# Kernel optimization log

Hardware: AMD Instinct MI355X
Metric: run time of the kernel (lower is better)

The kernel has to match this reference:

```python
import jax, jax.numpy as jnp
from jax import lax
import numpy as np

THRESHOLD = 1.25
CURRENT_DECAY = 0.25
VOLTAGE_DECAY = 0.03
TAU_GRAD = 0.03
SCALE_GRAD = 3.0


@jax.custom_vjp
def spike_fn(v):
    # Heaviside spike on membrane voltage (threshold already subtracted)
    return (v >= 0.0).astype(v.dtype)

def _spike_fwd(v):
    return spike_fn(v), v

def _spike_bwd(v, g):
    # slayer-style exponential surrogate gradient around threshold
    surrogate = SCALE_GRAD * jnp.exp(-jnp.abs(v) / TAU_GRAD)
    return (g * surrogate,)

spike_fn.defvjp(_spike_fwd, _spike_bwd)


def cuba_dense(x, v_w, g_w, delay):
    """x: [B, C_in, T] spikes -> [B, C_out, T] spikes.
    Weight-normalized dense synapse + CUBA leaky-integrate-and-fire scan + axonal delay."""
    # weight norm: W = g * v / ||v||_row
    norm = jnp.sqrt(jnp.sum(v_w * v_w, axis=1, keepdims=True))
    W = g_w[:, None] * v_w / norm                       # [O, C]
    z = jnp.einsum('bct,oc->bot', x, W)                 # synaptic current input [B, O, T]
    B, O, T = z.shape
    zT = jnp.transpose(z, (2, 0, 1))                    # [T, B, O]

    def step(carry, zt):
        cur, vol = carry
        cur = cur * (1.0 - CURRENT_DECAY) + zt
        vol = vol * (1.0 - VOLTAGE_DECAY) + cur
        s = spike_fn(vol - THRESHOLD)
        vol = vol * (1.0 - s)                           # reset to zero on spike
        return (cur, vol), s

    init = (jnp.zeros((B, O), z.dtype), jnp.zeros((B, O), z.dtype))
    _, sT = lax.scan(step, init, zT)                    # [T, B, O]
    s = jnp.transpose(sT, (1, 2, 0))                    # [B, O, T]

    # per-neuron integer axonal delay: out[b,n,t] = s[b,n,t-d_n]
    t_idx = jnp.arange(T)[None, :] - delay[:, None]     # [O, T]
    valid = (t_idx >= 0)
    gathered = s[:, jnp.arange(O)[:, None], jnp.clip(t_idx, 0, T - 1)]
    return jnp.where(valid[None, :, :], gathered, jnp.zeros((), s.dtype))


def setup_inputs() -> dict:
    key = jax.random.key(0)
    ks = jax.random.split(key, 10)
    B, C, T = 32, 34 * 34 * 2, 300
    spike = (jax.random.uniform(ks[0], (B, C, T)) < 0.1).astype(jnp.float32)
    v1 = jax.random.normal(ks[1], (512, C), jnp.float32) * 0.1
    g1 = jax.random.uniform(ks[2], (512,), jnp.float32) + 0.5
    v2 = jax.random.normal(ks[3], (512, 512), jnp.float32) * 0.1
    g2 = jax.random.uniform(ks[4], (512,), jnp.float32) + 0.5
    v3 = jax.random.normal(ks[5], (10, 512), jnp.float32) * 0.1
    g3 = jax.random.uniform(ks[6], (10,), jnp.float32) + 0.5
    d1 = jax.random.randint(ks[7], (512,), 0, 8, jnp.int32)
    d2 = jax.random.randint(ks[8], (512,), 0, 8, jnp.int32)
    d3 = jax.random.randint(ks[9], (10,), 0, 8, jnp.int32)
    return {"spike": spike, "v1": v1, "g1": g1, "v2": v2, "g2": g2,
            "v3": v3, "g3": g3, "d1": d1, "d2": d2, "d3": d3}


def reference(spike, v1, g1, v2, g2, v3, g3, d1, d2, d3):
    s1 = cuba_dense(spike, v1, g1, d1)
    s2 = cuba_dense(s1, v2, g2, d2)
    s3 = cuba_dense(s2, v3, g3, d3)
    counts = jnp.stack([jnp.mean(s1), jnp.mean(s2), jnp.mean(s3)]).reshape(1, -1)
    return s3, counts
```

## Files before the change

kernel.cpp:

```cpp
#include <hip/hip_runtime.h>

#define B_   32
#define T_   300
#define C1_  2312
#define O1_  512
#define O2_  512
#define O3_  10
#define M_   (B_*T_)
#define KSPLIT_ 1152


__global__ void calc_f(const float* __restrict__ v, const float* __restrict__ g,
                       double* __restrict__ f, int O, int C) {
    int o = blockIdx.x;
    const float* row = v + (size_t)o * C;
    double s = 0.0;
    for (int c = threadIdx.x; c < C; c += blockDim.x) {
        double x = (double)row[c];
        s += x * x;
    }
    for (int off = 32; off; off >>= 1) s += __shfl_down(s, off);
    __shared__ double wsum[4];
    int lane = threadIdx.x & 63, wv = threadIdx.x >> 6;
    if (lane == 0) wsum[wv] = s;
    __syncthreads();
    if (threadIdx.x == 0) {
        double tot = 0.0;
        for (int i = 0; i < (int)(blockDim.x >> 6); ++i) tot += wsum[i];
        f[o] = (double)g[o] / sqrt(tot);
    }
}

__global__ void transpose_scale(const float* __restrict__ v, const double* __restrict__ f,
                                double* __restrict__ wt, int O, int C, int ldo) {
    __shared__ double tile[32][33];
    int c0 = blockIdx.x * 32, o0 = blockIdx.y * 32;
    int tx = threadIdx.x, ty = threadIdx.y;
    for (int k = 0; k < 4; ++k) {
        int o = o0 + ty + k * 8, c = c0 + tx;
        double val = 0.0;
        if (o < O && c < C) val = (double)v[(size_t)o * C + c] * f[o];
        tile[ty + k * 8][tx] = val;
    }
    __syncthreads();
    for (int k = 0; k < 4; ++k) {
        int c = c0 + ty + k * 8, o = o0 + tx;
        if (c < C && o < O) wt[(size_t)c * ldo + o] = tile[tx][ty + k * 8];
    }
}

__global__ void build_bits(const float* __restrict__ X, unsigned* __restrict__ bits) {
    size_t idx = (size_t)blockIdx.x * 256 + threadIdx.x;
    if (idx >= (size_t)B_ * C1_ * 10) return;
    int t32 = (int)(idx % 10);
    size_t bc = idx / 10;
    const float* src = X + bc * T_ + t32 * 32;
    int nq = (t32 == 9) ? 3 : 8;
    unsigned m = 0;
    for (int q = 0; q < nq; ++q) {
        float4 v = *(const float4*)(src + q * 4);
        if (v.x != 0.f) m |= 1u << (q * 4 + 0);
        if (v.y != 0.f) m |= 1u << (q * 4 + 1);
        if (v.z != 0.f) m |= 1u << (q * 4 + 2);
        if (v.w != 0.f) m |= 1u << (q * 4 + 3);
    }
    bits[idx] = m;
}

__global__ __launch_bounds__(256) void gemm1(const unsigned* __restrict__ Xbits,
                                             const double* __restrict__ Wt,
                                             double* __restrict__ Z) {
    __shared__ double Ws[16][256];
    int zb = blockIdx.z;
    int b = zb >> 1, khalf = zb & 1;
    int cbeg = khalf ? KSPLIT_ : 0;
    const int NT = khalf ? 73 : 72;
    int o0 = blockIdx.y * 256;
    int tb = blockIdx.x;
    int tid = threadIdx.x;
    int lane = tid & 63;
    int w8s = __builtin_amdgcn_readfirstlane((tid >> 6) << 3);
    double acc[8][4];
#pragma unroll
    for (int tj = 0; tj < 8; ++tj)
#pragma unroll
        for (int i = 0; i < 4; ++i) acc[tj][i] = 0.0;
    const unsigned* xbp = Xbits + (size_t)b * C1_ * 10 + tb;

    double2 wreg[8];
    unsigned mk[16], mkn[16];

    auto load_w = [&](int c0) {
#pragma unroll
        for (int h = 0; h < 8; ++h) {
            int idx = h * 256 + tid;
            int i = idx >> 7, od = (idx & 127) * 2;
            int c = c0 + i;
            double2 val; val.x = 0.0; val.y = 0.0;
            if (c < C1_) val = *(const double2*)(Wt + (size_t)c * O1_ + o0 + od);
            wreg[h] = val;
        }
    };
    auto load_m = [&](unsigned* dst, int c0) {
#pragma unroll
        for (int k = 0; k < 16; ++k) {
            int c = c0 + k;
            dst[k] = (c < C1_) ? xbp[(size_t)c * 10] : 0u;
        }
    };
    auto store_w = [&]() {
#pragma unroll
        for (int h = 0; h < 8; ++h) {
            int idx = h * 256 + tid;
            int i = idx >> 7, od = (idx & 127) * 2;
            *(double2*)(&Ws[i][od]) = wreg[h];
        }
    };

    load_w(cbeg);
    load_m(mk, cbeg);
    for (int tile = 0; tile < NT; ++tile) {
        store_w();
        __syncthreads();
        if (tile + 1 < NT) {
            int cn = cbeg + (tile + 1) * 16;
            load_w(cn);
            load_m(mkn, cn);
        }
#pragma unroll
        for (int k = 0; k < 16; ++k) {
            unsigned smk = (unsigned)__builtin_amdgcn_readfirstlane((int)mk[k]);
            unsigned soct = (smk >> w8s) & 0xffu;
            if (soct) {
                double wf[4];
#pragma unroll
                for (int i = 0; i < 4; ++i) wf[i] = Ws[k][lane + 64 * i];
#pragma unroll
                for (int tj = 0; tj < 8; ++tj) {
                    if (soct & (1u << tj)) {
#pragma unroll
                        for (int i = 0; i < 4; ++i) acc[tj][i] += wf[i];
                    }
                }
            }
        }
#pragma unroll
        for (int k = 0; k < 16; ++k) mk[k] = mkn[k];
        __syncthreads();
    }
#pragma unroll
    for (int tj = 0; tj < 8; ++tj) {
        int t = tb * 32 + w8s + tj;
        if (t < T_) {
            double* dst = Z + ((size_t)b * T_ + t) * O1_ + o0;
#pragma unroll
            for (int i = 0; i < 4; ++i)
                atomicAdd(&dst[lane + 64 * i], acc[tj][i]);
        }
    }
}

__global__ __launch_bounds__(256) void gemm2(const float* __restrict__ A,
                                             const double* __restrict__ Wt,
                                             double* __restrict__ Z) {
    __shared__ double Ws[16][128];
    __shared__ double As[64][17];
    int m0 = blockIdx.x * 64;
    int o0 = blockIdx.y * 128;
    int tid = threadIdx.x;
    int to = tid & 15, tm = tid >> 4;
    double acc[8][4];
#pragma unroll
    for (int i = 0; i < 8; ++i)
#pragma unroll
        for (int j = 0; j < 4; ++j) acc[i][j] = 0.0;
    for (int c0 = 0; c0 < 512; c0 += 16) {
        {
            int m = tid >> 2, ch = (tid & 3) * 4;
            float4 v = *(const float4*)(A + (size_t)(m0 + m) * 512 + c0 + ch);
            As[m][ch + 0] = (double)v.x; As[m][ch + 1] = (double)v.y;
            As[m][ch + 2] = (double)v.z; As[m][ch + 3] = (double)v.w;
        }
#pragma unroll
        for (int h = 0; h < 4; ++h) {
            int idx = h * 512 + tid * 2;
            int i = idx >> 7, o = idx & 127;
            *(double2*)(&Ws[i][o]) = *(const double2*)(Wt + (size_t)(c0 + i) * 512 + o0 + o);
        }
        __syncthreads();
#pragma unroll
        for (int k = 0; k < 16; ++k) {
            double wf[8], xf[4];
#pragma unroll
            for (int i = 0; i < 8; ++i) wf[i] = Ws[k][to + 16 * i];
#pragma unroll
            for (int j = 0; j < 4; ++j) xf[j] = As[tm * 4 + j][k];
#pragma unroll
            for (int i = 0; i < 8; ++i)
#pragma unroll
                for (int j = 0; j < 4; ++j) acc[i][j] = fma(wf[i], xf[j], acc[i][j]);
        }
        __syncthreads();
    }
#pragma unroll
    for (int j = 0; j < 4; ++j) {
        double* dst = Z + (size_t)(m0 + tm * 4 + j) * 512 + o0;
#pragma unroll
        for (int i = 0; i < 8; ++i) dst[to + 16 * i] = acc[i][j];
    }
}

__global__ __launch_bounds__(256) void gemm3(const float* __restrict__ A,
                                             const double* __restrict__ Wt,
                                             double* __restrict__ Z) {
    __shared__ double w[512 * 16];
    for (int e = threadIdx.x; e < 4096; e += 256)
        ((double2*)w)[e] = ((const double2*)Wt)[e];
    __syncthreads();
    int m = blockIdx.x * 256 + threadIdx.x;
    if (m >= M_) return;
    double acc[O3_];
#pragma unroll
    for (int o = 0; o < O3_; ++o) acc[o] = 0.0;
    const float4* Ar = (const float4*)(A + (size_t)m * 512);
    for (int cq = 0; cq < 128; ++cq) {
        float4 a = Ar[cq];
        float av[4] = {a.x, a.y, a.z, a.w};
#pragma unroll
        for (int u = 0; u < 4; ++u)
#pragma unroll
            for (int o = 0; o < O3_; ++o) acc[o] += (double)av[u] * w[(cq * 4 + u) * 16 + o];
    }
    double* dst = Z + (size_t)m * 16;
#pragma unroll
    for (int o = 0; o < O3_; ++o) dst[o] = acc[o];
}

__global__ void scan12(const double* __restrict__ Zin,
                       const int* __restrict__ delay,
                       float* __restrict__ Sout,
                       float* __restrict__ sumOut) {
    int blk = blockIdx.x;
    int o = (blk & 7) * 64 + threadIdx.x;
    int b = blk >> 3;
    const double* z = Zin + (size_t)b * T_ * O1_ + o;
    float* s = Sout + (size_t)b * T_ * O1_ + o;
    int d = delay[o];
    for (int t = 0; t < d; ++t) s[(size_t)t * O1_] = 0.f;
    double cur = 0.0, vol = 0.0;
    float cnt = 0.f;
    for (int t8 = 0; t8 < 296; t8 += 8) {
        double zb[8];
#pragma unroll
        for (int u = 0; u < 8; ++u) zb[u] = z[(size_t)(t8 + u) * O1_];
#pragma unroll
        for (int u = 0; u < 8; ++u) {
            int t = t8 + u;
            cur = cur * 0.75 + zb[u];
            vol = vol * 0.97 + cur;
            float sp = (vol >= 1.25) ? 1.f : 0.f;
            if (sp > 0.f) vol = 0.0;
            int tw = t + d;
            if (tw < T_) { s[(size_t)tw * O1_] = sp; cnt += sp; }
        }
    }
    {
        double zb[4];
#pragma unroll
        for (int u = 0; u < 4; ++u) zb[u] = z[(size_t)(296 + u) * O1_];
#pragma unroll
        for (int u = 0; u < 4; ++u) {
            int t = 296 + u;
            cur = cur * 0.75 + zb[u];
            vol = vol * 0.97 + cur;
            float sp = (vol >= 1.25) ? 1.f : 0.f;
            if (sp > 0.f) vol = 0.0;
            int tw = t + d;
            if (tw < T_) { s[(size_t)tw * O1_] = sp; cnt += sp; }
        }
    }
    for (int off = 32; off; off >>= 1) cnt += __shfl_down(cnt, off);
    if (threadIdx.x == 0) atomicAdd(sumOut, cnt);
}

__global__ void scan3(const double* __restrict__ Z3,
                      const int* __restrict__ d3,
                      float* __restrict__ out,
                      float* __restrict__ sumOut) {
    __shared__ double zt[T_ * 16];
    int b = blockIdx.x;
    const double2* src = (const double2*)(Z3 + (size_t)b * T_ * 16);
    for (int e = threadIdx.x; e < T_ * 8; e += 64)
        ((double2*)zt)[e] = src[e];
    __syncthreads();
    int o = threadIdx.x;
    if (o < O3_) {
        int d = d3[o];
        float* dst = out + (size_t)b * O3_ * T_ + (size_t)o * T_;
        for (int t = 0; t < d; ++t) dst[t] = 0.f;
        double cur = 0.0, vol = 0.0;
        float cnt = 0.f;
        for (int t = 0; t < T_; ++t) {
            cur = cur * 0.75 + zt[t * 16 + o];
            vol = vol * 0.97 + cur;
            float sp = (vol >= 1.25) ? 1.f : 0.f;
            if (sp > 0.f) vol = 0.0;
            int tw = t + d;
            if (tw < T_) { dst[tw] = sp; cnt += sp; }
        }
        atomicAdd(sumOut, cnt);
    }
}

__global__ void finalize(const float* __restrict__ sums, float* __restrict__ out) {
    if (threadIdx.x == 0) {
        out[0] = (float)((double)sums[0] / (double)(B_ * O1_ * T_));
        out[1] = (float)((double)sums[1] / (double)(B_ * O2_ * T_));
        out[2] = (float)((double)sums[2] / (double)(B_ * O3_ * T_));
    }
}

extern "C" void kernel_launch(void* const* d_in, const int* in_sizes, int n_in,
                              void* d_out, int out_size, void* d_ws, size_t ws_size,
                              hipStream_t stream) {
    const float* spike = (const float*)d_in[0];
    const float* v1 = (const float*)d_in[1];
    const float* g1 = (const float*)d_in[2];
    const float* v2 = (const float*)d_in[3];
    const float* g2 = (const float*)d_in[4];
    const float* v3 = (const float*)d_in[5];
    const float* g3 = (const float*)d_in[6];
    const int* d1 = (const int*)d_in[7];
    const int* d2 = (const int*)d_in[8];
    const int* d3 = (const int*)d_in[9];
    float* out = (float*)d_out;

    double* dw = (double*)d_ws;
    size_t off = 0;
    double* f1  = dw + off; off += 512;
    double* f2  = dw + off; off += 512;
    double* f3  = dw + off; off += 16;
    double* Wt1 = dw + off; off += (size_t)C1_ * O1_;
    double* Wt2 = dw + off; off += 512 * 512;
    double* Wt3 = dw + off; off += 512 * 16;
    double* zA  = dw + off; off += (size_t)M_ * 512;
    double* z3b = dw + off; off += (size_t)M_ * 16;
    float* fw = (float*)(dw + off);
    float* sB    = fw;
    float* sums  = fw + (size_t)M_ * 512;
    unsigned* Xbits = (unsigned*)(fw + (size_t)M_ * 512 + 4);
    (void)ws_size; (void)out_size; (void)in_sizes; (void)n_in;

    hipMemsetAsync(sums, 0, 4 * sizeof(float), stream);
    hipMemsetAsync(zA, 0, (size_t)M_ * 512 * sizeof(double), stream);

    build_bits<<<(B_ * C1_ * 10 + 255) / 256, 256, 0, stream>>>(spike, Xbits);

    calc_f<<<512, 256, 0, stream>>>(v1, g1, f1, O1_, C1_);
    calc_f<<<512, 256, 0, stream>>>(v2, g2, f2, O2_, O1_);
    calc_f<<<O3_, 256, 0, stream>>>(v3, g3, f3, O3_, O2_);

    transpose_scale<<<dim3((C1_ + 31) / 32, 16), dim3(32, 8), 0, stream>>>(v1, f1, Wt1, O1_, C1_, O1_);
    transpose_scale<<<dim3(16, 16), dim3(32, 8), 0, stream>>>(v2, f2, Wt2, O2_, O1_, O2_);
    transpose_scale<<<dim3(16, 1), dim3(32, 8), 0, stream>>>(v3, f3, Wt3, O3_, O2_, 16);

    gemm1<<<dim3(10, 2, B_ * 2), 256, 0, stream>>>(Xbits, Wt1, zA);
    scan12<<<256, 64, 0, stream>>>(zA, d1, sB, sums + 0);
    gemm2<<<dim3(M_ / 64, 4), 256, 0, stream>>>(sB, Wt2, zA);
    scan12<<<256, 64, 0, stream>>>(zA, d2, sB, sums + 1);
    gemm3<<<(M_ + 255) / 256, 256, 0, stream>>>(sB, Wt3, z3b);
    scan3<<<B_, 64, 0, stream>>>(z3b, d3, out, sums + 2);
    finalize<<<1, 64, 0, stream>>>(sums, out + (size_t)B_ * O3_ * T_);
}
```

Before: 854.2 us.

## Bit-pack layer-1 spikes and make gemm2 a sparse masked accumulation

The layer-1 scan now writes its spikes as 32-bit time masks per neuron instead of dense float rows. The second-layer GEMM reads these masks and, for each input channel and group of 8 timesteps, adds weight rows only where a spike bit is set. This replaces dense fp64 FMAs with conditional adds, mirroring the existing gemm1 design. It also software-pipelines the weight and mask loads across tiles, at the cost of wave-uniform branching and more register use.

```diff
diff --git a/kernel.cpp b/kernel.cpp
--- a/kernel.cpp
+++ b/kernel.cpp
@@ -160,53 +160,86 @@
     }
 }
 
-__global__ __launch_bounds__(256) void gemm2(const float* __restrict__ A,
+__global__ __launch_bounds__(256) void gemm2(const unsigned* __restrict__ Sbits,
                                              const double* __restrict__ Wt,
                                              double* __restrict__ Z) {
-    __shared__ double Ws[16][128];
-    __shared__ double As[64][17];
-    int m0 = blockIdx.x * 64;
-    int o0 = blockIdx.y * 128;
+    __shared__ double Ws[16][256];
+    int b  = blockIdx.z;
+    int o0 = blockIdx.y * 256;
+    int tb = blockIdx.x;
     int tid = threadIdx.x;
-    int to = tid & 15, tm = tid >> 4;
+    int lane = tid & 63;
+    int w8s = __builtin_amdgcn_readfirstlane((tid >> 6) << 3);
     double acc[8][4];
 #pragma unroll
-    for (int i = 0; i < 8; ++i)
-#pragma unroll
-        for (int j = 0; j < 4; ++j) acc[i][j] = 0.0;
-    for (int c0 = 0; c0 < 512; c0 += 16) {
-        {
-            int m = tid >> 2, ch = (tid & 3) * 4;
-            float4 v = *(const float4*)(A + (size_t)(m0 + m) * 512 + c0 + ch);
-            As[m][ch + 0] = (double)v.x; As[m][ch + 1] = (double)v.y;
-            As[m][ch + 2] = (double)v.z; As[m][ch + 3] = (double)v.w;
-        }
-#pragma unroll
-        for (int h = 0; h < 4; ++h) {
-            int idx = h * 512 + tid * 2;
-            int i = idx >> 7, o = idx & 127;
-            *(double2*)(&Ws[i][o]) = *(const double2*)(Wt + (size_t)(c0 + i) * 512 + o0 + o);
-        }
+    for (int tj = 0; tj < 8; ++tj)
+#pragma unroll
+        for (int i = 0; i < 4; ++i) acc[tj][i] = 0.0;
+    const unsigned* xbp = Sbits + (size_t)b * 512 * 10 + tb;
+
+    double2 wreg[8];
+    unsigned mk[16], mkn[16];
+
+    auto load_w = [&](int c0) {
+#pragma unroll
+        for (int h = 0; h < 8; ++h) {
+            int idx = h * 256 + tid;
+            int i = idx >> 7, od = (idx & 127) * 2;
+            wreg[h] = *(const double2*)(Wt + (size_t)(c0 + i) * 512 + o0 + od);
+        }
+    };
+    auto load_m = [&](unsigned* dst, int c0) {
+#pragma unroll
+        for (int k = 0; k < 16; ++k) dst[k] = xbp[(size_t)(c0 + k) * 10];
+    };
+    auto store_w = [&]() {
+#pragma unroll
+        for (int h = 0; h < 8; ++h) {
+            int idx = h * 256 + tid;
+            int i = idx >> 7, od = (idx & 127) * 2;
+            *(double2*)(&Ws[i][od]) = wreg[h];
+        }
+    };
+
+    load_w(0);
+    load_m(mk, 0);
+    for (int tile = 0; tile < 32; ++tile) {
+        store_w();
         __syncthreads();
+        if (tile + 1 < 32) {
+            int cn = (tile + 1) * 16;
+            load_w(cn);
+            load_m(mkn, cn);
+        }
 #pragma unroll
         for (int k = 0; k < 16; ++k) {
-            double wf[8], xf[4];
-#pragma unroll
-            for (int i = 0; i < 8; ++i) wf[i] = Ws[k][to + 16 * i];
-#pragma unroll
-            for (int j = 0; j < 4; ++j) xf[j] = As[tm * 4 + j][k];
-#pragma unroll
-            for (int i = 0; i < 8; ++i)
-#pragma unroll
-                for (int j = 0; j < 4; ++j) acc[i][j] = fma(wf[i], xf[j], acc[i][j]);
-        }
+            unsigned smk = (unsigned)__builtin_amdgcn_readfirstlane((int)mk[k]);
+            unsigned soct = (smk >> w8s) & 0xffu;
+            if (soct) {
+                double wf[4];
+#pragma unroll
+                for (int i = 0; i < 4; ++i) wf[i] = Ws[k][lane + 64 * i];
+#pragma unroll
+                for (int tj = 0; tj < 8; ++tj) {
+                    if (soct & (1u << tj)) {
+#pragma unroll
+                        for (int i = 0; i < 4; ++i) acc[tj][i] += wf[i];
+                    }
+                }
+            }
+        }
+#pragma unroll
+        for (int k = 0; k < 16; ++k) mk[k] = mkn[k];
         __syncthreads();
     }
 #pragma unroll
-    for (int j = 0; j < 4; ++j) {
-        double* dst = Z + (size_t)(m0 + tm * 4 + j) * 512 + o0;
-#pragma unroll
-        for (int i = 0; i < 8; ++i) dst[to + 16 * i] = acc[i][j];
+    for (int tj = 0; tj < 8; ++tj) {
+        int t = tb * 32 + w8s + tj;
+        if (t < T_) {
+            double* dst = Z + ((size_t)b * T_ + t) * O1_ + o0;
+#pragma unroll
+            for (int i = 0; i < 4; ++i) dst[lane + 64 * i] = acc[tj][i];
+        }
     }
 }
 
@@ -239,6 +272,7 @@
 __global__ void scan12(const double* __restrict__ Zin,
                        const int* __restrict__ delay,
                        float* __restrict__ Sout,
+                       unsigned* __restrict__ bitsOut,
                        float* __restrict__ sumOut) {
     int blk = blockIdx.x;
     int o = (blk & 7) * 64 + threadIdx.x;
@@ -246,7 +280,11 @@
     const double* z = Zin + (size_t)b * T_ * O1_ + o;
     float* s = Sout + (size_t)b * T_ * O1_ + o;
     int d = delay[o];
-    for (int t = 0; t < d; ++t) s[(size_t)t * O1_] = 0.f;
+    bool emitBits = (bitsOut != nullptr);
+    unsigned* bout = emitBits ? (bitsOut + ((size_t)b * 512 + o) * 10) : nullptr;
+    unsigned mcur = 0; int mi = 0;
+    if (!emitBits)
+        for (int t = 0; t < d; ++t) s[(size_t)t * O1_] = 0.f;
     double cur = 0.0, vol = 0.0;
     float cnt = 0.f;
     for (int t8 = 0; t8 < 296; t8 += 8) {
@@ -261,7 +299,16 @@
             float sp = (vol >= 1.25) ? 1.f : 0.f;
             if (sp > 0.f) vol = 0.0;
             int tw = t + d;
-            if (tw < T_) { s[(size_t)tw * O1_] = sp; cnt += sp; }
+            if (tw < T_) {
+                if (emitBits) {
+                    int w = tw >> 5;
+                    if (w != mi) { bout[mi] = mcur; mcur = 0; mi = w; }
+                    if (sp > 0.f) mcur |= 1u << (tw & 31);
+                } else {
+                    s[(size_t)tw * O1_] = sp;
+                }
+                cnt += sp;
+            }
         }
     }
     {
@@ -276,9 +323,19 @@
             float sp = (vol >= 1.25) ? 1.f : 0.f;
             if (sp > 0.f) vol = 0.0;
             int tw = t + d;
-            if (tw < T_) { s[(size_t)tw * O1_] = sp; cnt += sp; }
-        }
-    }
+            if (tw < T_) {
+                if (emitBits) {
+                    int w = tw >> 5;
+                    if (w != mi) { bout[mi] = mcur; mcur = 0; mi = w; }
+                    if (sp > 0.f) mcur |= 1u << (tw & 31);
+                } else {
+                    s[(size_t)tw * O1_] = sp;
+                }
+                cnt += sp;
+            }
+        }
+    }
+    if (emitBits) bout[mi] = mcur;
     for (int off = 32; off; off >>= 1) cnt += __shfl_down(cnt, off);
     if (threadIdx.x == 0) atomicAdd(sumOut, cnt);
 }
@@ -349,6 +406,7 @@
     float* sB    = fw;
     float* sums  = fw + (size_t)M_ * 512;
     unsigned* Xbits = (unsigned*)(fw + (size_t)M_ * 512 + 4);
+    unsigned* Sbits = Xbits + (size_t)B_ * C1_ * 10;
     (void)ws_size; (void)out_size; (void)in_sizes; (void)n_in;
 
     hipMemsetAsync(sums, 0, 4 * sizeof(float), stream);
@@ -365,9 +423,9 @@
     transpose_scale<<<dim3(16, 1), dim3(32, 8), 0, stream>>>(v3, f3, Wt3, O3_, O2_, 16);
 
     gemm1<<<dim3(10, 2, B_ * 2), 256, 0, stream>>>(Xbits, Wt1, zA);
-    scan12<<<256, 64, 0, stream>>>(zA, d1, sB, sums + 0);
-    gemm2<<<dim3(M_ / 64, 4), 256, 0, stream>>>(sB, Wt2, zA);
-    scan12<<<256, 64, 0, stream>>>(zA, d2, sB, sums + 1);
+    scan12<<<256, 64, 0, stream>>>(zA, d1, sB, Sbits, sums + 0);
+    gemm2<<<dim3(10, 2, B_), 256, 0, stream>>>(Sbits, Wt2, zA);
+    scan12<<<256, 64, 0, stream>>>(zA, d2, sB, nullptr, sums + 1);
     gemm3<<<(M_ + 255) / 256, 256, 0, stream>>>(sB, Wt3, z3b);
     scan3<<<B_, 64, 0, stream>>>(z3b, d3, out, sums + 2);
     finalize<<<1, 64, 0, stream>>>(sums, out + (size_t)B_ * O3_ * T_);
```

After: 922.6 us. 8.0% more time.
